# Kernel optimization log

Hardware: AMD Instinct MI355X
Metric: run time of the kernel (lower is better)

## Reference

```python
import jax, jax.numpy as jnp
import numpy as np


def setup_inputs() -> dict:
    key = jax.random.key(0)
    contour = jax.random.uniform(key, (200, 2), dtype=jnp.float32)  # coords in [0,1]
    return {"contour": contour, "size": 384}


def reference(contour, size):
    S = size
    eps = 1e-05
    k = 100000.0  # forward hardcodes k, ignoring self.k
    # mesh: (S^2, 1, 2), normalized pixel coordinates (torch.meshgrid default 'ij')
    grid = jnp.stack(jnp.meshgrid(jnp.arange(S), jnp.arange(S), indexing="ij"), axis=-1)
    mesh = (grid.reshape(-1, 2).astype(jnp.float32) / S)[:, None, :]
    diff = contour[None, :, :] - mesh                      # (S^2, N, 2)
    norm_diff = jnp.linalg.norm(diff, axis=-1)             # (S^2, N)
    min_diff = jnp.min(norm_diff, axis=1).reshape(S, S)    # distance to nearest vertex
    roll_diff = jnp.roll(diff, -1, axis=1)                 # next vertex diff
    # torch.roll(roll_diff, 1, dims=2) on a size-2 axis swaps x/y components
    cross = diff * roll_diff[..., ::-1]                    # (S^2, N, 2)
    sign = jnp.tanh(k * (cross[..., 1] - cross[..., 0]))   # smooth sign of 2D cross
    nd = jnp.clip(norm_diff, eps)
    nr = jnp.clip(jnp.linalg.norm(roll_diff, axis=-1), eps)
    cos_ang = jnp.clip(jnp.sum(diff * roll_diff, axis=-1) / (nd * nr), -1.0 + eps, 1.0 - eps)
    angles = jnp.arccos(cos_ang)                           # (S^2, N)
    winding = jnp.sum(sign * angles, axis=1) / (2.0 * jnp.pi)  # (S^2,)
    resize = winding.reshape(1, S, S)
    prod = resize * min_diff                               # (1, S, S)
    dmap = (prod / jnp.max(prod))[None]                    # (1, 1, S, S)
    return dmap
```

## Files before the change

### kernel.cpp

```cpp
#include <hip/hip_runtime.h>
#include <math.h>


#define INV_2PI 0.15915494309189535f
#define TWO_PI  6.28318530717958648f
#define PI_F    3.14159265358979323846f
#define HPI_F   1.57079632679489662f
#define KK2     200000.0f
#define CTHR    9e-5f

__device__ __forceinline__ float atan01(float q) {
    const float z = q * q;
    float p = fmaf(z,  0.0208351f, -0.0851330f);
    p = fmaf(z, p,  0.1801410f);
    p = fmaf(z, p, -0.3302995f);
    p = fmaf(z, p,  0.9998660f);
    return q * p;
}

__device__ __forceinline__ float corr_term(float ax_, float ay_, float bx_,
                                           float by_, float px, float py,
                                           float V) {
    const float dxc = ax_ - px, dyc = ay_ - py;
    const float dxn = bx_ - px, dyn = by_ - py;
    const float dot = fmaf(dxc, dxn, dyc * dyn);
    const float ay = fabsf(V), ax = fabsf(dot);
    const float mn = fminf(ax, ay), mx = fmaxf(ax, ay);
    const float q  = mn * __builtin_amdgcn_rcpf(fmaxf(mx, 1e-30f));
    float an = atan01(q);
    an = (ay > ax)    ? (HPI_F - an) : an;
    an = (dot < 0.0f) ? (PI_F - an)  : an;
    const float e = __expf(ay * -KK2);
    const float t = (1.0f - e) * __builtin_amdgcn_rcpf(1.0f + e);
    return (1.0f - t) * copysignf(an, -V);
}

__global__ void __launch_bounds__(256)
scan_kernel(const float2* __restrict__ c, int N, int S, float invS,
            float* __restrict__ wbuf) {
    __shared__ int   D[512];
    __shared__ float WC[512];
    __shared__ int   lst[16];
    __shared__ int   lcnt;

    const int tid = threadIdx.x;
    const int col = blockIdx.x;
    const float px = (float)col * invS;
    const float Sf = (float)S;

    for (int t = tid; t < 512; t += 256) { D[t] = 0; WC[t] = 0.0f; }
    if (tid == 0) lcnt = 0;
    __syncthreads();

    for (int n = tid; n < N; n += 256) {
        const float2 a = c[n];
        const float2 b = c[(n + 1 < N) ? (n + 1) : 0];
        const float EX = b.x - a.x;
        const float EY = b.y - a.y;
        const float Cc = a.x * b.y - a.y * b.x;
        const float W  = fmaf(-px, EY, Cc);

        const float ylo = fminf(a.y, b.y);
        const float yhi = fmaxf(a.y, b.y);
        const int s = (b.y > a.y) ? 1 : -1;
        int ja = (int)ceilf(ylo * Sf);
        int jb = (int)ceilf(yhi * Sf);
        ja = max(ja, 0); jb = min(jb, S);
        if (ja < jb) {
            const float Ga = (float)s * fmaf(EX, (float)ja * invS, W);
            const float Gb = (float)s * fmaf(EX, (float)(jb - 1) * invS, W);
            int j0 = ja, j1 = jb;
            if (Ga > 0.0f && Gb > 0.0f) {
            } else if (!(Ga > 0.0f) && !(Gb > 0.0f)) {
                j1 = j0;
            } else {
                const float r = -W / EX;
                const float rj = fminf(fmaxf(r * Sf, -1.0f), 386.0f);
                int jm = (int)ceilf(rj);
                jm = min(max(jm, ja), jb);
                if (Ga > 0.0f) j1 = jm; else j0 = jm;
            }
            if (j0 < j1) {
                atomicAdd(&D[j0],  s);
                atomicAdd(&D[j1], -s);
            }
        }

        const float aEX = fabsf(EX);
        if (aEX < 1e-12f) {
            if (fabsf(W) < CTHR) {
                const int k = atomicAdd(&lcnt, 1);
                if (k < 16) lst[k] = n;
            }
        } else {
            const float r  = -W / EX;
            const float dl = CTHR / aEX;
            float flo = (r - dl) * Sf;
            float fhi = (r + dl) * Sf;
            if (fhi >= 0.0f && flo <= Sf - 1.0f) {
                flo = fmaxf(flo, 0.0f);
                fhi = fminf(fhi, Sf - 1.0f);
                const int jl = (int)ceilf(flo);
                const int jh = (int)floorf(fhi);
                if (jh - jl > 12) {
                    const int k = atomicAdd(&lcnt, 1);
                    if (k < 16) lst[k] = n;
                } else {
                    for (int j = jl; j <= jh; ++j) {
                        const float py = (float)j * invS;
                        const float V = fmaf(EX, py, W);
                        if (fabsf(V) < CTHR)
                            atomicAdd(&WC[j],
                                      corr_term(a.x, a.y, b.x, b.y, px, py, V));
                    }
                }
            }
        }
    }
    __syncthreads();

    const int L = min(lcnt, 16);
    for (int k = 0; k < L; ++k) {
        const int n = lst[k];
        const float2 a = c[n];
        const float2 b = c[(n + 1 < N) ? (n + 1) : 0];
        const float EX = b.x - a.x;
        const float EY = b.y - a.y;
        const float W  = fmaf(-px, EY, a.x * b.y - a.y * b.x);
        for (int j = tid; j < S; j += 256) {
            const float py = (float)j * invS;
            const float V = fmaf(EX, py, W);
            if (fabsf(V) < CTHR)
                atomicAdd(&WC[j], corr_term(a.x, a.y, b.x, b.y, px, py, V));
        }
    }
    __syncthreads();

    #pragma unroll
    for (int off = 1; off < 512; off <<= 1) {
        const int j0 = tid, j1 = tid + 256;
        const int v0 = D[j0] + ((j0 >= off) ? D[j0 - off] : 0);
        const int v1 = D[j1] + ((j1 >= off) ? D[j1 - off] : 0);
        __syncthreads();
        D[j0] = v0; D[j1] = v1;
        __syncthreads();
    }

    for (int j = tid; j < S; j += 256)
        wbuf[col * S + j] = fmaf(-TWO_PI, (float)D[j], -WC[j]);
}

__global__ void __launch_bounds__(256)
prod_kernel(const float2* __restrict__ c, int N, int S, float invS,
            const float* __restrict__ wbuf, float* __restrict__ out,
            float* __restrict__ bmax) {
    const int tid = threadIdx.x;
    const int lane = tid & 63;
    const int wid  = tid >> 6;
    const int p = blockIdx.x * 256 + tid;
    const int i = p / S, j = p - i * S;
    const float px = (float)i * invS, py = (float)j * invS;

    float m0 = 1e30f, m1 = 1e30f, m2 = 1e30f, m3 = 1e30f;
    int n = 0;
    for (; n + 4 <= N; n += 4) {
        const float2 v0 = c[n],     v1 = c[n + 1];
        const float2 v2 = c[n + 2], v3 = c[n + 3];
        float dx, dy;
        dx = v0.x - px; dy = v0.y - py; m0 = fminf(m0, fmaf(dx, dx, dy * dy));
        dx = v1.x - px; dy = v1.y - py; m1 = fminf(m1, fmaf(dx, dx, dy * dy));
        dx = v2.x - px; dy = v2.y - py; m2 = fminf(m2, fmaf(dx, dx, dy * dy));
        dx = v3.x - px; dy = v3.y - py; m3 = fminf(m3, fmaf(dx, dx, dy * dy));
    }
    for (; n < N; ++n) {
        const float2 v = c[n];
        const float dx = v.x - px, dy = v.y - py;
        m0 = fminf(m0, fmaf(dx, dx, dy * dy));
    }
    const float minn = fminf(fminf(m0, m1), fminf(m2, m3));
    const float prod = (wbuf[p] * INV_2PI) * __builtin_amdgcn_sqrtf(minn);
    out[p] = prod;

    float v = prod;
    #pragma unroll
    for (int off = 32; off >= 1; off >>= 1)
        v = fmaxf(v, __shfl_down(v, off, 64));
    __shared__ float s_red[4];
    if (lane == 0) s_red[wid] = v;
    __syncthreads();
    if (tid == 0)
        bmax[blockIdx.x] = fmaxf(fmaxf(s_red[0], s_red[1]),
                                 fmaxf(s_red[2], s_red[3]));
}

__global__ void __launch_bounds__(256)
normalize_kernel(float4* __restrict__ out4, const float* __restrict__ bmax,
                 int nmax, int total4) {
    const int tid  = threadIdx.x;
    const int lane = tid & 63;
    const int wid  = tid >> 6;

    float m = -INFINITY;
    for (int t = tid; t < nmax; t += 256) m = fmaxf(m, bmax[t]);
    #pragma unroll
    for (int off = 32; off >= 1; off >>= 1)
        m = fmaxf(m, __shfl_down(m, off, 64));
    __shared__ float sm[4];
    if (lane == 0) sm[wid] = m;
    __syncthreads();
    m = fmaxf(fmaxf(sm[0], sm[1]), fmaxf(sm[2], sm[3]));
    const float inv = 1.0f / m;

    const int idx = blockIdx.x * 256 + tid;
    if (idx < total4) {
        float4 v = out4[idx];
        v.x *= inv; v.y *= inv; v.z *= inv; v.w *= inv;
        out4[idx] = v;
    }
}

extern "C" void kernel_launch(void* const* d_in, const int* in_sizes, int n_in,
                              void* d_out, int out_size, void* d_ws, size_t ws_size,
                              hipStream_t stream) {
    const float2* contour = (const float2*)d_in[0];
    const int N = in_sizes[0] / 2;
    const int S = (int)(sqrt((double)out_size) + 0.5);
    const float invS = 1.0f / (float)S;
    float* out  = (float*)d_out;
    float* bmax = (float*)d_ws;
    float* wbuf = (float*)((char*)d_ws + 16384);

    scan_kernel<<<S, 256, 0, stream>>>(contour, N, S, invS, wbuf);

    const int total  = S * S;
    const int pblocks = total / 256;
    prod_kernel<<<pblocks, 256, 0, stream>>>(contour, N, S, invS, wbuf,
                                             out, bmax);

    const int total4  = total / 4;
    const int nblocks = (total4 + 255) / 256;
    normalize_kernel<<<nblocks, 256, 0, stream>>>((float4*)out, bmax,
                                                  pblocks, total4);
}
```

Baseline: 69.21 us.

## Cull contour vertices per 16x16 tile before nearest-vertex search

The pixel-product kernel now maps each block to a 16x16 pixel tile. It computes the tile centre's nearest-vertex distance, keeps only vertices within that distance plus the tile's half-diagonal in shared memory, and searches just that candidate list per pixel. This replaces the full O(N) scan per pixel with a short list, at the cost of two extra passes over the contour per block, block syncs and shared atomics. The per-pixel work is now data-dependent, and the code assumes S is a multiple of 16.

```diff
diff --git a/kernel.cpp b/kernel.cpp
--- a/kernel.cpp
+++ b/kernel.cpp
@@ -154,30 +154,61 @@
 prod_kernel(const float2* __restrict__ c, int N, int S, float invS,
             const float* __restrict__ wbuf, float* __restrict__ out,
             float* __restrict__ bmax) {
-    const int tid = threadIdx.x;
+    __shared__ float2 sv[256];
+    __shared__ int    scnt;
+    __shared__ float  s_cd[4];
+    __shared__ float  s_red[4];
+
+    const int tid  = threadIdx.x;
     const int lane = tid & 63;
     const int wid  = tid >> 6;
-    const int p = blockIdx.x * 256 + tid;
-    const int i = p / S, j = p - i * S;
+
+    const int nbx = S >> 4;
+    const int bi = blockIdx.x / nbx;
+    const int bj = blockIdx.x - bi * nbx;
+    const int i = (bi << 4) + (tid >> 4);
+    const int j = (bj << 4) + (tid & 15);
     const float px = (float)i * invS, py = (float)j * invS;
 
-    float m0 = 1e30f, m1 = 1e30f, m2 = 1e30f, m3 = 1e30f;
-    int n = 0;
-    for (; n + 4 <= N; n += 4) {
-        const float2 v0 = c[n],     v1 = c[n + 1];
-        const float2 v2 = c[n + 2], v3 = c[n + 3];
-        float dx, dy;
-        dx = v0.x - px; dy = v0.y - py; m0 = fminf(m0, fmaf(dx, dx, dy * dy));
-        dx = v1.x - px; dy = v1.y - py; m1 = fminf(m1, fmaf(dx, dx, dy * dy));
-        dx = v2.x - px; dy = v2.y - py; m2 = fminf(m2, fmaf(dx, dx, dy * dy));
-        dx = v3.x - px; dy = v3.y - py; m3 = fminf(m3, fmaf(dx, dx, dy * dy));
-    }
-    for (; n < N; ++n) {
+    const float cx = ((float)(bi << 4) + 7.5f) * invS;
+    const float cy = ((float)(bj << 4) + 7.5f) * invS;
+
+    float cmin = 1e30f;
+    for (int n = tid; n < N; n += 256) {
         const float2 v = c[n];
+        const float dx = v.x - cx, dy = v.y - cy;
+        cmin = fminf(cmin, fmaf(dx, dx, dy * dy));
+    }
+    #pragma unroll
+    for (int off = 32; off >= 1; off >>= 1)
+        cmin = fminf(cmin, __shfl_down(cmin, off, 64));
+    if (lane == 0) s_cd[wid] = cmin;
+    if (tid == 0) scnt = 0;
+    __syncthreads();
+    const float minc = fminf(fminf(s_cd[0], s_cd[1]), fminf(s_cd[2], s_cd[3]));
+
+    const float T  = sqrtf(minc) + 0.0560f;
+    const float T2 = T * T;
+
+    for (int n = tid; n < N; n += 256) {
+        const float2 v = c[n];
+        const float dx = v.x - cx, dy = v.y - cy;
+        if (fmaf(dx, dx, dy * dy) <= T2) {
+            const int k = atomicAdd(&scnt, 1);
+            sv[k] = v;
+        }
+    }
+    __syncthreads();
+
+    const int M = scnt;
+    float minn = 1e30f;
+    for (int k = 0; k < M; ++k) {
+        const float2 v = sv[k];
         const float dx = v.x - px, dy = v.y - py;
-        m0 = fminf(m0, fmaf(dx, dx, dy * dy));
-    }
-    const float minn = fminf(fminf(m0, m1), fminf(m2, m3));
+        minn = fminf(minn, fmaf(dx, dx, dy * dy));
+    }
+
+    const int p = i * S + j;
     const float prod = (wbuf[p] * INV_2PI) * __builtin_amdgcn_sqrtf(minn);
     out[p] = prod;
 
@@ -185,7 +216,6 @@
     #pragma unroll
     for (int off = 32; off >= 1; off >>= 1)
         v = fmaxf(v, __shfl_down(v, off, 64));
-    __shared__ float s_red[4];
     if (lane == 0) s_red[wid] = v;
     __syncthreads();
     if (tid == 0)
```

After: 64.21 us, median of 2. 7.2% less time.
